# Kernel optimization log

Measured on AMD Instinct MI355X. Metric: run time of the kernel, lower is better.

The kernel has to match this reference:

```python
import jax, jax.numpy as jnp
import numpy as np

EPS = 1e-5  # BatchNorm2d default eps


def _deform_conv(x, offset, W_def, b_def, K):
    # torchvision.ops.DeformConv2d, stride=1, dilation=1, padding=K//2, groups=1
    B, C, H, W = x.shape
    KK = K * K
    pad = K // 2
    # offset channels ordered (y, x) per kernel tap: [B, KK, 2, H, W]
    off = offset.reshape(B, KK, 2, H, W)
    ky = (jnp.arange(KK) // K).astype(x.dtype)
    kx = (jnp.arange(KK) % K).astype(x.dtype)
    base_y = jnp.arange(H, dtype=x.dtype)[None, :, None] - pad + ky[:, None, None]  # [KK,H,1]
    base_x = jnp.arange(W, dtype=x.dtype)[None, None, :] - pad + kx[:, None, None]  # [KK,1,W]
    py = off[:, :, 0] + base_y[None]  # [B,KK,H,W] sampling rows
    px = off[:, :, 1] + base_x[None]  # [B,KK,H,W] sampling cols
    y0 = jnp.floor(py)
    x0 = jnp.floor(px)
    wy = py - y0
    wx = px - x0
    xf = x.reshape(B, C, H * W)

    def corner(iy, ix, w):
        valid = ((iy >= 0) & (iy < H) & (ix >= 0) & (ix < W)).astype(x.dtype)
        idx = jnp.clip(iy, 0, H - 1).astype(jnp.int32) * W + jnp.clip(ix, 0, W - 1).astype(jnp.int32)
        g = jnp.take_along_axis(xf, idx.reshape(B, 1, KK * H * W), axis=2)
        return g.reshape(B, C, KK, H, W) * (w * valid)[:, None]

    sampled = (corner(y0, x0, (1 - wy) * (1 - wx))
               + corner(y0, x0 + 1, (1 - wy) * wx)
               + corner(y0 + 1, x0, wy * (1 - wx))
               + corner(y0 + 1, x0 + 1, wy * wx))  # [B,C,KK,H,W]
    out = jnp.einsum('bckhw,ock->bohw', sampled, W_def.reshape(W_def.shape[0], C, KK))
    return out + b_def[None, :, None, None]


def reference(x, W_off, b_off, W_def, b_def, W_cat, b_cat, gamma, beta):
    K = W_def.shape[-1]
    # 3x3 offset-generating conv, padding=1
    offset = jax.lax.conv_general_dilated(
        x, W_off, (1, 1), ((1, 1), (1, 1)),
        dimension_numbers=('NCHW', 'OIHW', 'NCHW')) + b_off[None, :, None, None]
    y1 = _deform_conv(x, offset, W_def, b_def, K)
    # 1x1 conv
    y = jnp.einsum('bchw,oc->bohw', y1, W_cat) + b_cat[None, :, None, None]
    # BatchNorm2d in training mode (batch statistics, biased var)
    mean = y.mean(axis=(0, 2, 3))
    var = y.var(axis=(0, 2, 3))
    yn = (y - mean[None, :, None, None]) * jax.lax.rsqrt(var + EPS)[None, :, None, None]
    out = jax.nn.relu(gamma[None, :, None, None] * yn + beta[None, :, None, None])
    return out + x


def setup_inputs() -> dict:
    key = jax.random.key(0)
    ks = jax.random.split(key, 5)
    B, C, H, W, K = 4, 64, 192, 192, 3
    return {
        'x': jax.random.normal(ks[0], (B, C, H, W), dtype=jnp.float32),
        'W_off': jax.random.normal(ks[1], (2 * K * K, C, 3, 3), dtype=jnp.float32) * 0.02,
        'b_off': jnp.zeros((2 * K * K,), dtype=jnp.float32),
        'W_def': jax.random.normal(ks[2], (C, C, K, K), dtype=jnp.float32) * (1.0 / np.sqrt(C * K * K)),
        'b_def': jnp.zeros((C,), dtype=jnp.float32),
        'W_cat': jax.random.normal(ks[3], (C, C), dtype=jnp.float32) * (1.0 / np.sqrt(C)),
        'b_cat': jnp.zeros((C,), dtype=jnp.float32),
        'gamma': jnp.ones((C,), dtype=jnp.float32),
        'beta': jnp.zeros((C,), dtype=jnp.float32),
    }
```

## Files before the change

kernel.cpp:

```cpp
#include <hip/hip_runtime.h>
#include <math.h>

constexpr int Hh  = 192;
constexpr int Ww  = 192;
constexpr int HWp = Hh * Ww;
constexpr int Cc  = 64;
constexpr int Bb  = 4;
constexpr int KK  = 9;
constexpr int OFFC = 18;
constexpr int PXB = 32;
constexpr int NBPX = HWp / PXB;
constexpr int KSD = (Cc * KK) / 32;
constexpr int KSC = Cc / 32;
constexpr int NIT = KK * PXB;
constexpr int SLOTS = 64;

using bf16x8 = __attribute__((ext_vector_type(8))) short;
using f32x4  = __attribute__((ext_vector_type(4))) float;

static __device__ __forceinline__ unsigned short f2bf(float f) {
    unsigned int u = __float_as_uint(f);
    u += 0x7fff + ((u >> 16) & 1);
    return (unsigned short)(u >> 16);
}
static __device__ __forceinline__ float bf2f(unsigned short u) {
    return __uint_as_float((unsigned)u << 16);
}

__global__ __launch_bounds__(256)
void k_xpose(const float* __restrict__ x, unsigned short* __restrict__ xcl) {
    __shared__ unsigned short tile[64][66];
    int b   = blockIdx.x / (HWp / 64);
    int px0 = (blockIdx.x % (HWp / 64)) * 64;
    int t = threadIdx.x;
    #pragma unroll
    for (int r = 0; r < 4; ++r) {
        int c = r * 16 + (t >> 4), px4 = (t & 15) * 4;
        float4 v = *(const float4*)(x + ((size_t)b * Cc + c) * HWp + px0 + px4);
        tile[c][px4 + 0] = f2bf(v.x);
        tile[c][px4 + 1] = f2bf(v.y);
        tile[c][px4 + 2] = f2bf(v.z);
        tile[c][px4 + 3] = f2bf(v.w);
    }
    __syncthreads();
    #pragma unroll
    for (int r = 0; r < 4; ++r) {
        int pxl = r * 16 + (t >> 4), c4 = (t & 15) * 4;
        ushort4 u;
        u.x = tile[c4 + 0][pxl];
        u.y = tile[c4 + 1][pxl];
        u.z = tile[c4 + 2][pxl];
        u.w = tile[c4 + 3][pxl];
        *(ushort4*)(xcl + ((size_t)b * HWp + px0 + pxl) * Cc + c4) = u;
    }
}

__global__ __launch_bounds__(256)
void k_wprep(const float* __restrict__ Wdef, const float* __restrict__ Wcat,
             const float* __restrict__ Woff,
             unsigned short* __restrict__ Fd, unsigned short* __restrict__ Fc,
             unsigned short* __restrict__ Fo) {
    int i = blockIdx.x * 256 + threadIdx.x;
    if (i < 4 * KSD * 64 * 8) {
        int r = i & 7, lane = (i >> 3) & 63, ks = (i >> 9) % KSD, ot = (i >> 9) / KSD;
        int o  = ot * 16 + (lane & 15);
        int kp = ks * 32 + ((lane >> 4) << 3) + r;
        int kk = kp >> 6, c = kp & 63;
        Fd[i] = f2bf(Wdef[o * (Cc * KK) + c * KK + kk]);
    }
    int j = i - 4 * KSD * 64 * 8;
    if (j >= 0 && j < 4 * KSC * 64 * 8) {
        int r = j & 7, lane = (j >> 3) & 63, ks = (j >> 9) & 1, ot = j >> 10;
        int o = ot * 16 + (lane & 15);
        int c = ks * 32 + ((lane >> 4) << 3) + r;
        Fc[j] = f2bf(Wcat[o * Cc + c]);
    }
    int m = j - 4 * KSC * 64 * 8;
    if (m >= 0 && m < 2 * KSD * 64 * 8) {
        int r = m & 7, lane = (m >> 3) & 63, ks = (m >> 9) % KSD, ot = (m >> 9) / KSD;
        int o  = ot * 16 + (lane & 15);
        int kp = ks * 32 + ((lane >> 4) << 3) + r;
        int kk = kp >> 6, c = kp & 63;
        Fo[m] = (o < OFFC) ? f2bf(Woff[o * (Cc * KK) + c * KK + kk]) : 0;
    }
}

__global__ __launch_bounds__(256)
void k_fused(const unsigned short* __restrict__ xcl,
             const unsigned short* __restrict__ Fo, const float* __restrict__ boff,
             const unsigned short* __restrict__ Fd, const float* __restrict__ bdef,
             const unsigned short* __restrict__ Fc, const float* __restrict__ bcat,
             float* __restrict__ y, float* __restrict__ psum) {
    __shared__ __align__(16) unsigned char s_buf[PXB * Cc * KK * 2];
    __shared__ __align__(16) unsigned char s_y1[PXB * Cc * 2];
    __shared__ float s_off[PXB][OFFC];
    __shared__ __align__(16) int s_pp[NIT * 8];

    const int t = threadIdx.x;
    const int lane = t & 63, wv = t >> 6;
    const int klane = lane >> 4;
    const int c4 = (lane & 15) * 4;
    int wg = blockIdx.x;
    const int slot = wg & (SLOTS - 1);
    wg = (wg & 7) * (Bb * NBPX / 8) + (wg >> 3);
    const int b   = wg / NBPX;
    const int px0 = (wg % NBPX) * PXB;
    const int h   = px0 / Ww;
    const int w0  = px0 % Ww;
    const unsigned short* xb = xcl + (size_t)b * HWp * Cc;

    #pragma unroll
    for (int it = 0; it < NIT / 16; ++it) {
        int item = it * 16 + wv * 4 + klane;
        int kk = item >> 5, pxl = item & 31;
        int ky = (kk * 11) >> 5, kx = kk - ky * 3;
        int row = h + ky - 1;
        int col = w0 + pxl + kx - 1;
        ushort4 u = {0, 0, 0, 0};
        if (row >= 0 && row < Hh && col >= 0 && col < Ww)
            u = *(const ushort4*)(xb + (size_t)(row * Ww + col) * Cc + c4);
        unsigned addr = (unsigned)pxl * (Cc * KK * 2)
                      + ((((unsigned)(kk * 64 + c4)) * 2) ^ ((unsigned)(pxl & 7) << 4));
        *(ushort4*)(s_buf + addr) = u;
    }
    __syncthreads();

    {
        const int pxt = wv & 1, oto = wv >> 1;
        const unsigned swzA = (unsigned)(lane & 7) << 4;
        const unsigned rA = ((unsigned)(lane & 15) + (unsigned)pxt * 16) * (Cc * KK * 2);
        f32x4 a = {0.f, 0.f, 0.f, 0.f};
        const bf16x8* Bo = (const bf16x8*)Fo + (size_t)oto * KSD * 64;
        #pragma unroll 3
        for (int ks = 0; ks < KSD; ++ks) {
            unsigned cb = ((unsigned)(ks * 64 + klane * 16)) ^ swzA;
            bf16x8 af = *(const bf16x8*)(s_buf + rA + cb);
            a = __builtin_amdgcn_mfma_f32_16x16x32_bf16(af, Bo[ks * 64 + lane], a, 0, 0, 0);
        }
        int oc = oto * 16 + (lane & 15);
        if (oc < OFFC) {
            float bv = boff[oc];
            #pragma unroll
            for (int r = 0; r < 4; ++r)
                s_off[pxt * 16 + klane * 4 + r][oc] = a[r] + bv;
        }
    }
    __syncthreads();

    for (int i = t; i < NIT; i += 256) {
        int kk = i >> 5, pxl = i & 31;
        int ky = (kk * 11) >> 5, kx = kk - ky * 3;
        float py  = s_off[pxl][kk * 2]     + (float)(h - 1 + ky);
        float pxf = s_off[pxl][kk * 2 + 1] + (float)(w0 + pxl - 1 + kx);
        float fy0 = floorf(py), fx0 = floorf(pxf);
        float wy = py - fy0, wx = pxf - fx0;
        int iy0 = (int)fy0, ix0 = (int)fx0, iy1 = iy0 + 1, ix1 = ix0 + 1;
        float v00 = (iy0 >= 0 && iy0 < Hh && ix0 >= 0 && ix0 < Ww) ? 1.f : 0.f;
        float v01 = (iy0 >= 0 && iy0 < Hh && ix1 >= 0 && ix1 < Ww) ? 1.f : 0.f;
        float v10 = (iy1 >= 0 && iy1 < Hh && ix0 >= 0 && ix0 < Ww) ? 1.f : 0.f;
        float v11 = (iy1 >= 0 && iy1 < Hh && ix1 >= 0 && ix1 < Ww) ? 1.f : 0.f;
        int cy0 = min(max(iy0, 0), Hh - 1), cy1 = min(max(iy1, 0), Hh - 1);
        int cx0 = min(max(ix0, 0), Ww - 1), cx1 = min(max(ix1, 0), Ww - 1);
        int* pp = &s_pp[i * 8];
        pp[0] = (cy0 * Ww + cx0) * (Cc * 2);
        pp[1] = (cy0 * Ww + cx1) * (Cc * 2);
        pp[2] = (cy1 * Ww + cx0) * (Cc * 2);
        pp[3] = (cy1 * Ww + cx1) * (Cc * 2);
        pp[4] = __float_as_int((1.f - wy) * (1.f - wx) * v00);
        pp[5] = __float_as_int((1.f - wy) * wx * v01);
        pp[6] = __float_as_int(wy * (1.f - wx) * v10);
        pp[7] = __float_as_int(wy * wx * v11);
    }
    __syncthreads();

    const unsigned char* xbB = (const unsigned char*)xb + (size_t)c4 * 2;
    #pragma unroll 2
    for (int it = 0; it < NIT / 16; ++it) {
        int item = it * 16 + wv * 4 + klane;
        int kk = item >> 5, pxl = item & 31;
        const int* pp = &s_pp[item * 8];
        int4   idx = *(const int4*)pp;
        float4 wt  = *(const float4*)(pp + 4);
        ushort4 u00 = *(const ushort4*)(xbB + idx.x);
        ushort4 u01 = *(const ushort4*)(xbB + idx.y);
        ushort4 u10 = *(const ushort4*)(xbB + idx.z);
        ushort4 u11 = *(const ushort4*)(xbB + idx.w);
        float v0 = wt.x * bf2f(u00.x) + wt.y * bf2f(u01.x) + wt.z * bf2f(u10.x) + wt.w * bf2f(u11.x);
        float v1 = wt.x * bf2f(u00.y) + wt.y * bf2f(u01.y) + wt.z * bf2f(u10.y) + wt.w * bf2f(u11.y);
        float v2 = wt.x * bf2f(u00.z) + wt.y * bf2f(u01.z) + wt.z * bf2f(u10.z) + wt.w * bf2f(u11.z);
        float v3 = wt.x * bf2f(u00.w) + wt.y * bf2f(u01.w) + wt.z * bf2f(u10.w) + wt.w * bf2f(u11.w);
        ushort4 o4;
        o4.x = f2bf(v0); o4.y = f2bf(v1); o4.z = f2bf(v2); o4.w = f2bf(v3);
        unsigned addr = (unsigned)pxl * (Cc * KK * 2)
                      + ((((unsigned)(kk * 64 + c4)) * 2) ^ ((unsigned)(pxl & 7) << 4));
        *(ushort4*)(s_buf + addr) = o4;
    }
    __syncthreads();

    const int ot = wv;
    const unsigned swzA = (unsigned)(lane & 7) << 4;
    const unsigned rA0  = (unsigned)(lane & 15) * (Cc * KK * 2);
    const unsigned rA1  = rA0 + 16u * (Cc * KK * 2);
    f32x4 acc0 = {0.f, 0.f, 0.f, 0.f}, acc1 = {0.f, 0.f, 0.f, 0.f};
    const bf16x8* Bd = (const bf16x8*)Fd + (size_t)ot * KSD * 64;
    #pragma unroll 3
    for (int ks = 0; ks < KSD; ++ks) {
        unsigned cb = ((unsigned)(ks * 64 + klane * 16)) ^ swzA;
        bf16x8 a0 = *(const bf16x8*)(s_buf + rA0 + cb);
        bf16x8 a1 = *(const bf16x8*)(s_buf + rA1 + cb);
        bf16x8 bd = Bd[ks * 64 + lane];
        acc0 = __builtin_amdgcn_mfma_f32_16x16x32_bf16(a0, bd, acc0, 0, 0, 0);
        acc1 = __builtin_amdgcn_mfma_f32_16x16x32_bf16(a1, bd, acc1, 0, 0, 0);
    }
    const int o = ot * 16 + (lane & 15);
    {
        float bv = bdef[o];
        unsigned colb = (unsigned)o * 2;
        #pragma unroll
        for (int r = 0; r < 4; ++r) {
            int row0 = klane * 4 + r, row1 = row0 + 16;
            unsigned sw = (unsigned)(row0 & 7) << 4;
            *(unsigned short*)(s_y1 + row0 * (Cc * 2) + (colb ^ sw)) = f2bf(acc0[r] + bv);
            *(unsigned short*)(s_y1 + row1 * (Cc * 2) + (colb ^ sw)) = f2bf(acc1[r] + bv);
        }
    }
    __syncthreads();

    f32x4 c0 = {0.f, 0.f, 0.f, 0.f}, c1 = {0.f, 0.f, 0.f, 0.f};
    const bf16x8* Bc = (const bf16x8*)Fc + (size_t)ot * KSC * 64;
    const unsigned rY0 = (unsigned)(lane & 15) * (Cc * 2);
    const unsigned rY1 = rY0 + 16u * (Cc * 2);
    #pragma unroll
    for (int ks = 0; ks < KSC; ++ks) {
        unsigned cb = ((unsigned)(ks * 64 + klane * 16)) ^ swzA;
        bf16x8 a0 = *(const bf16x8*)(s_y1 + rY0 + cb);
        bf16x8 a1 = *(const bf16x8*)(s_y1 + rY1 + cb);
        bf16x8 bc = Bc[ks * 64 + lane];
        c0 = __builtin_amdgcn_mfma_f32_16x16x32_bf16(a0, bc, c0, 0, 0, 0);
        c1 = __builtin_amdgcn_mfma_f32_16x16x32_bf16(a1, bc, c1, 0, 0, 0);
    }

    float vals[8];
    {
        float bcv = bcat[o];
        #pragma unroll
        for (int r = 0; r < 4; ++r) { vals[r] = c0[r] + bcv; vals[4 + r] = c1[r] + bcv; }
        float s1 = 0.f, s2 = 0.f;
        #pragma unroll
        for (int j = 0; j < 8; ++j) { s1 += vals[j]; s2 += vals[j] * vals[j]; }
        s1 += __shfl_xor(s1, 16); s1 += __shfl_xor(s1, 32);
        s2 += __shfl_xor(s2, 16); s2 += __shfl_xor(s2, 32);
        if (klane == 0) {
            atomicAdd(&psum[o * SLOTS + slot], s1);
            atomicAdd(&psum[Cc * SLOTS + o * SLOTS + slot], s2);
        }
    }

    __syncthreads();
    {
        unsigned orow = (unsigned)o * (PXB * 4);
        unsigned sw   = (unsigned)(o & 7) << 4;
        #pragma unroll
        for (int r = 0; r < 4; ++r) {
            int p0 = klane * 4 + r, p1 = p0 + 16;
            *(float*)(s_buf + orow + (((unsigned)p0 * 4) ^ sw)) = vals[r];
            *(float*)(s_buf + orow + (((unsigned)p1 * 4) ^ sw)) = vals[4 + r];
        }
    }
    __syncthreads();
    float* yb = y + (size_t)b * Cc * HWp + px0;
    #pragma unroll
    for (int it = 0; it < 2; ++it) {
        int oo = it * 32 + (t >> 3), pxq = t & 7;
        float4 v = *(const float4*)(s_buf + (unsigned)oo * (PXB * 4)
                                    + (((unsigned)pxq * 16) ^ ((unsigned)(oo & 7) << 4)));
        *(float4*)(yb + (size_t)oo * HWp + pxq * 4) = v;
    }
}

__global__ __launch_bounds__(64)
void k_stats_final(const float* __restrict__ psum, float* __restrict__ stats) {
    int c = threadIdx.x;
    double t1 = 0.0, t2 = 0.0;
    for (int s = 0; s < SLOTS; ++s) {
        t1 += (double)psum[c * SLOTS + s];
        t2 += (double)psum[Cc * SLOTS + c * SLOTS + s];
    }
    double n = (double)(Bb * HWp);
    double mean = t1 / n;
    double var  = t2 / n - mean * mean;
    stats[c]      = (float)mean;
    stats[Cc + c] = (float)(1.0 / sqrt(var + 1e-5));
}

__global__ __launch_bounds__(256)
void k_apply(const float4* __restrict__ y, const float4* __restrict__ x,
             const float* __restrict__ stats, const float* __restrict__ gamma,
             const float* __restrict__ beta, float4* __restrict__ out) {
    int idx = blockIdx.x * 256 + threadIdx.x;
    int c = (idx / (HWp / 4)) % Cc;
    float mean = stats[c], inv = stats[Cc + c];
    float g = gamma[c], bt = beta[c];
    float4 yv = y[idx], xv = x[idx], o;
    o.x = fmaxf(g * ((yv.x - mean) * inv) + bt, 0.f) + xv.x;
    o.y = fmaxf(g * ((yv.y - mean) * inv) + bt, 0.f) + xv.y;
    o.z = fmaxf(g * ((yv.z - mean) * inv) + bt, 0.f) + xv.z;
    o.w = fmaxf(g * ((yv.w - mean) * inv) + bt, 0.f) + xv.w;
    out[idx] = o;
}

extern "C" void kernel_launch(void* const* d_in, const int* in_sizes, int n_in,
                              void* d_out, int out_size, void* d_ws, size_t ws_size,
                              hipStream_t stream) {
    const float* x     = (const float*)d_in[0];
    const float* Woff  = (const float*)d_in[1];
    const float* boff  = (const float*)d_in[2];
    const float* Wdef  = (const float*)d_in[3];
    const float* bdef  = (const float*)d_in[4];
    const float* Wcat  = (const float*)d_in[5];
    const float* bcat  = (const float*)d_in[6];
    const float* gamma = (const float*)d_in[7];
    const float* beta  = (const float*)d_in[8];
    float* out = (float*)d_out;

    float* ws    = (float*)d_ws;
    float* ybuf  = ws;
    float* stats = ybuf + (size_t)Bb * Cc * HWp;
    float* psum  = stats + 128;
    unsigned short* Fd  = (unsigned short*)(psum + 2 * Cc * SLOTS);
    unsigned short* Fc  = Fd + 4 * KSD * 64 * 8;
    unsigned short* Fo  = Fc + 4 * KSC * 64 * 8;
    unsigned short* xcl = Fo + 2 * KSD * 64 * 8;

    hipMemsetAsync(psum, 0, 2 * Cc * SLOTS * sizeof(float), stream);
    k_xpose<<<dim3(Bb * (HWp / 64)), dim3(256), 0, stream>>>(x, xcl);
    k_wprep<<<dim3((4 * KSD * 64 * 8 + 4 * KSC * 64 * 8 + 2 * KSD * 64 * 8 + 255) / 256),
              dim3(256), 0, stream>>>(Wdef, Wcat, Woff, Fd, Fc, Fo);
    k_fused<<<dim3(Bb * NBPX), dim3(256), 0, stream>>>(xcl, Fo, boff, Fd, bdef, Fc, bcat, ybuf, psum);
    k_stats_final<<<dim3(1), dim3(64), 0, stream>>>(psum, stats);
    k_apply<<<dim3(Bb * Cc * HWp / 4 / 256), dim3(256), 0, stream>>>(
        (const float4*)ybuf, (const float4*)x, stats, gamma, beta, (float4*)out);
}
```

Baseline: 217.5 us.

## Merge prep kernels, widen fused block to 512 threads, store intermediate y in bf16

Three changes at once. The transpose, weight-prep and psum-zeroing launches are merged into one kernel, dropping a memset and a launch. The fused kernel now runs 8 waves per block, so each wave does one 16x16 output tile instead of two. The pre-BatchNorm activation y is written and read as bf16 instead of fp32, halving that round-trip through memory. The trade-offs are lower precision in the normalised output, since the stats still come from fp32 values, and higher register and occupancy pressure at 512 threads.

```diff
diff --git a/kernel.cpp b/kernel.cpp
--- a/kernel.cpp
+++ b/kernel.cpp
@@ -15,6 +15,10 @@
 constexpr int NIT = KK * PXB;
 constexpr int SLOTS = 64;
 
+constexpr int NXP = Bb * (HWp / 64);
+constexpr int NWP = (4 * KSD * 64 * 8 + 4 * KSC * 64 * 8 + 2 * KSD * 64 * 8) / 256;
+constexpr int NZP = (2 * Cc * SLOTS / 4) / 256;
+
 using bf16x8 = __attribute__((ext_vector_type(8))) short;
 using f32x4  = __attribute__((ext_vector_type(4))) float;
 
@@ -28,69 +32,74 @@
 }
 
 __global__ __launch_bounds__(256)
-void k_xpose(const float* __restrict__ x, unsigned short* __restrict__ xcl) {
+void k_prep(const float* __restrict__ x, const float* __restrict__ Wdef,
+            const float* __restrict__ Wcat, const float* __restrict__ Woff,
+            unsigned short* __restrict__ xcl, unsigned short* __restrict__ Fd,
+            unsigned short* __restrict__ Fc, unsigned short* __restrict__ Fo,
+            float* __restrict__ psum) {
     __shared__ unsigned short tile[64][66];
-    int b   = blockIdx.x / (HWp / 64);
-    int px0 = (blockIdx.x % (HWp / 64)) * 64;
-    int t = threadIdx.x;
-    #pragma unroll
-    for (int r = 0; r < 4; ++r) {
-        int c = r * 16 + (t >> 4), px4 = (t & 15) * 4;
-        float4 v = *(const float4*)(x + ((size_t)b * Cc + c) * HWp + px0 + px4);
-        tile[c][px4 + 0] = f2bf(v.x);
-        tile[c][px4 + 1] = f2bf(v.y);
-        tile[c][px4 + 2] = f2bf(v.z);
-        tile[c][px4 + 3] = f2bf(v.w);
-    }
-    __syncthreads();
-    #pragma unroll
-    for (int r = 0; r < 4; ++r) {
-        int pxl = r * 16 + (t >> 4), c4 = (t & 15) * 4;
-        ushort4 u;
-        u.x = tile[c4 + 0][pxl];
-        u.y = tile[c4 + 1][pxl];
-        u.z = tile[c4 + 2][pxl];
-        u.w = tile[c4 + 3][pxl];
-        *(ushort4*)(xcl + ((size_t)b * HWp + px0 + pxl) * Cc + c4) = u;
-    }
-}
-
-__global__ __launch_bounds__(256)
-void k_wprep(const float* __restrict__ Wdef, const float* __restrict__ Wcat,
-             const float* __restrict__ Woff,
-             unsigned short* __restrict__ Fd, unsigned short* __restrict__ Fc,
-             unsigned short* __restrict__ Fo) {
-    int i = blockIdx.x * 256 + threadIdx.x;
-    if (i < 4 * KSD * 64 * 8) {
-        int r = i & 7, lane = (i >> 3) & 63, ks = (i >> 9) % KSD, ot = (i >> 9) / KSD;
-        int o  = ot * 16 + (lane & 15);
-        int kp = ks * 32 + ((lane >> 4) << 3) + r;
-        int kk = kp >> 6, c = kp & 63;
-        Fd[i] = f2bf(Wdef[o * (Cc * KK) + c * KK + kk]);
-    }
-    int j = i - 4 * KSD * 64 * 8;
-    if (j >= 0 && j < 4 * KSC * 64 * 8) {
-        int r = j & 7, lane = (j >> 3) & 63, ks = (j >> 9) & 1, ot = j >> 10;
-        int o = ot * 16 + (lane & 15);
-        int c = ks * 32 + ((lane >> 4) << 3) + r;
-        Fc[j] = f2bf(Wcat[o * Cc + c]);
-    }
-    int m = j - 4 * KSC * 64 * 8;
-    if (m >= 0 && m < 2 * KSD * 64 * 8) {
-        int r = m & 7, lane = (m >> 3) & 63, ks = (m >> 9) % KSD, ot = (m >> 9) / KSD;
-        int o  = ot * 16 + (lane & 15);
-        int kp = ks * 32 + ((lane >> 4) << 3) + r;
-        int kk = kp >> 6, c = kp & 63;
-        Fo[m] = (o < OFFC) ? f2bf(Woff[o * (Cc * KK) + c * KK + kk]) : 0;
-    }
-}
-
-__global__ __launch_bounds__(256)
+    const int bid = blockIdx.x;
+    const int t = threadIdx.x;
+    if (bid < NXP) {
+        int b   = bid / (HWp / 64);
+        int px0 = (bid % (HWp / 64)) * 64;
+        #pragma unroll
+        for (int r = 0; r < 4; ++r) {
+            int c = r * 16 + (t >> 4), px4 = (t & 15) * 4;
+            float4 v = *(const float4*)(x + ((size_t)b * Cc + c) * HWp + px0 + px4);
+            tile[c][px4 + 0] = f2bf(v.x);
+            tile[c][px4 + 1] = f2bf(v.y);
+            tile[c][px4 + 2] = f2bf(v.z);
+            tile[c][px4 + 3] = f2bf(v.w);
+        }
+        __syncthreads();
+        #pragma unroll
+        for (int r = 0; r < 4; ++r) {
+            int pxl = r * 16 + (t >> 4), c4 = (t & 15) * 4;
+            ushort4 u;
+            u.x = tile[c4 + 0][pxl];
+            u.y = tile[c4 + 1][pxl];
+            u.z = tile[c4 + 2][pxl];
+            u.w = tile[c4 + 3][pxl];
+            *(ushort4*)(xcl + ((size_t)b * HWp + px0 + pxl) * Cc + c4) = u;
+        }
+    } else if (bid < NXP + NWP) {
+        int i = (bid - NXP) * 256 + t;
+        if (i < 4 * KSD * 64 * 8) {
+            int r = i & 7, lane = (i >> 3) & 63, ks = (i >> 9) % KSD, ot = (i >> 9) / KSD;
+            int o  = ot * 16 + (lane & 15);
+            int kp = ks * 32 + ((lane >> 4) << 3) + r;
+            int kk = kp >> 6, c = kp & 63;
+            Fd[i] = f2bf(Wdef[o * (Cc * KK) + c * KK + kk]);
+        }
+        int j = i - 4 * KSD * 64 * 8;
+        if (j >= 0 && j < 4 * KSC * 64 * 8) {
+            int r = j & 7, lane = (j >> 3) & 63, ks = (j >> 9) & 1, ot = j >> 10;
+            int o = ot * 16 + (lane & 15);
+            int c = ks * 32 + ((lane >> 4) << 3) + r;
+            Fc[j] = f2bf(Wcat[o * Cc + c]);
+        }
+        int m = j - 4 * KSC * 64 * 8;
+        if (m >= 0 && m < 2 * KSD * 64 * 8) {
+            int r = m & 7, lane = (m >> 3) & 63, ks = (m >> 9) % KSD, ot = (m >> 9) / KSD;
+            int o  = ot * 16 + (lane & 15);
+            int kp = ks * 32 + ((lane >> 4) << 3) + r;
+            int kk = kp >> 6, c = kp & 63;
+            Fo[m] = (o < OFFC) ? f2bf(Woff[o * (Cc * KK) + c * KK + kk]) : 0;
+        }
+    } else {
+        int j = (bid - NXP - NWP) * 256 + t;
+        float4 z = {0.f, 0.f, 0.f, 0.f};
+        ((float4*)psum)[j] = z;
+    }
+}
+
+__global__ __launch_bounds__(512)
 void k_fused(const unsigned short* __restrict__ xcl,
              const unsigned short* __restrict__ Fo, const float* __restrict__ boff,
              const unsigned short* __restrict__ Fd, const float* __restrict__ bdef,
              const unsigned short* __restrict__ Fc, const float* __restrict__ bcat,
-             float* __restrict__ y, float* __restrict__ psum) {
+             unsigned short* __restrict__ y, float* __restrict__ psum) {
     __shared__ __align__(16) unsigned char s_buf[PXB * Cc * KK * 2];
     __shared__ __align__(16) unsigned char s_y1[PXB * Cc * 2];
     __shared__ float s_off[PXB][OFFC];
@@ -98,7 +107,7 @@
 
     const int t = threadIdx.x;
     const int lane = t & 63, wv = t >> 6;
-    const int klane = lane >> 4;
+    const int klane = (lane >> 4) & 3;
     const int c4 = (lane & 15) * 4;
     int wg = blockIdx.x;
     const int slot = wg & (SLOTS - 1);
@@ -110,8 +119,8 @@
     const unsigned short* xb = xcl + (size_t)b * HWp * Cc;
 
     #pragma unroll
-    for (int it = 0; it < NIT / 16; ++it) {
-        int item = it * 16 + wv * 4 + klane;
+    for (int it = 0; it < NIT / 32; ++it) {
+        int item = it * 32 + wv * 4 + klane;
         int kk = item >> 5, pxl = item & 31;
         int ky = (kk * 11) >> 5, kx = kk - ky * 3;
         int row = h + ky - 1;
@@ -125,15 +134,15 @@
     }
     __syncthreads();
 
-    {
-        const int pxt = wv & 1, oto = wv >> 1;
-        const unsigned swzA = (unsigned)(lane & 7) << 4;
+    if (wv < 4) {
+        const int oto = wv >> 1, pxt = wv & 1;
+        const unsigned swz = (unsigned)(lane & 7) << 4;
         const unsigned rA = ((unsigned)(lane & 15) + (unsigned)pxt * 16) * (Cc * KK * 2);
         f32x4 a = {0.f, 0.f, 0.f, 0.f};
         const bf16x8* Bo = (const bf16x8*)Fo + (size_t)oto * KSD * 64;
         #pragma unroll 3
         for (int ks = 0; ks < KSD; ++ks) {
-            unsigned cb = ((unsigned)(ks * 64 + klane * 16)) ^ swzA;
+            unsigned cb = ((unsigned)(ks * 64 + klane * 16)) ^ swz;
             bf16x8 af = *(const bf16x8*)(s_buf + rA + cb);
             a = __builtin_amdgcn_mfma_f32_16x16x32_bf16(af, Bo[ks * 64 + lane], a, 0, 0, 0);
         }
@@ -147,7 +156,8 @@
     }
     __syncthreads();
 
-    for (int i = t; i < NIT; i += 256) {
+    if (t < NIT) {
+        int i = t;
         int kk = i >> 5, pxl = i & 31;
         int ky = (kk * 11) >> 5, kx = kk - ky * 3;
         float py  = s_off[pxl][kk * 2]     + (float)(h - 1 + ky);
@@ -174,9 +184,9 @@
     __syncthreads();
 
     const unsigned char* xbB = (const unsigned char*)xb + (size_t)c4 * 2;
-    #pragma unroll 2
-    for (int it = 0; it < NIT / 16; ++it) {
-        int item = it * 16 + wv * 4 + klane;
+    #pragma unroll 3
+    for (int it = 0; it < NIT / 32; ++it) {
+        int item = it * 32 + wv * 4 + klane;
         int kk = item >> 5, pxl = item & 31;
         const int* pp = &s_pp[item * 8];
         int4   idx = *(const int4*)pp;
@@ -197,20 +207,17 @@
     }
     __syncthreads();
 
-    const int ot = wv;
+    const int ot = wv >> 1, pxt = wv & 1;
     const unsigned swzA = (unsigned)(lane & 7) << 4;
-    const unsigned rA0  = (unsigned)(lane & 15) * (Cc * KK * 2);
-    const unsigned rA1  = rA0 + 16u * (Cc * KK * 2);
-    f32x4 acc0 = {0.f, 0.f, 0.f, 0.f}, acc1 = {0.f, 0.f, 0.f, 0.f};
+    const unsigned rA = ((unsigned)(lane & 15) + (unsigned)pxt * 16) * (Cc * KK * 2);
+    f32x4 acc = {0.f, 0.f, 0.f, 0.f};
     const bf16x8* Bd = (const bf16x8*)Fd + (size_t)ot * KSD * 64;
     #pragma unroll 3
     for (int ks = 0; ks < KSD; ++ks) {
         unsigned cb = ((unsigned)(ks * 64 + klane * 16)) ^ swzA;
-        bf16x8 a0 = *(const bf16x8*)(s_buf + rA0 + cb);
-        bf16x8 a1 = *(const bf16x8*)(s_buf + rA1 + cb);
+        bf16x8 a0 = *(const bf16x8*)(s_buf + rA + cb);
         bf16x8 bd = Bd[ks * 64 + lane];
-        acc0 = __builtin_amdgcn_mfma_f32_16x16x32_bf16(a0, bd, acc0, 0, 0, 0);
-        acc1 = __builtin_amdgcn_mfma_f32_16x16x32_bf16(a1, bd, acc1, 0, 0, 0);
+        acc = __builtin_amdgcn_mfma_f32_16x16x32_bf16(a0, bd, acc, 0, 0, 0);
     }
     const int o = ot * 16 + (lane & 15);
     {
@@ -218,36 +225,32 @@
         unsigned colb = (unsigned)o * 2;
         #pragma unroll
         for (int r = 0; r < 4; ++r) {
-            int row0 = klane * 4 + r, row1 = row0 + 16;
-            unsigned sw = (unsigned)(row0 & 7) << 4;
-            *(unsigned short*)(s_y1 + row0 * (Cc * 2) + (colb ^ sw)) = f2bf(acc0[r] + bv);
-            *(unsigned short*)(s_y1 + row1 * (Cc * 2) + (colb ^ sw)) = f2bf(acc1[r] + bv);
-        }
-    }
-    __syncthreads();
-
-    f32x4 c0 = {0.f, 0.f, 0.f, 0.f}, c1 = {0.f, 0.f, 0.f, 0.f};
+            int row = pxt * 16 + klane * 4 + r;
+            unsigned sw = (unsigned)((klane * 4 + r) & 7) << 4;
+            *(unsigned short*)(s_y1 + row * (Cc * 2) + (colb ^ sw)) = f2bf(acc[r] + bv);
+        }
+    }
+    __syncthreads();
+
+    f32x4 cacc = {0.f, 0.f, 0.f, 0.f};
     const bf16x8* Bc = (const bf16x8*)Fc + (size_t)ot * KSC * 64;
-    const unsigned rY0 = (unsigned)(lane & 15) * (Cc * 2);
-    const unsigned rY1 = rY0 + 16u * (Cc * 2);
+    const unsigned rY = ((unsigned)(lane & 15) + (unsigned)pxt * 16) * (Cc * 2);
     #pragma unroll
     for (int ks = 0; ks < KSC; ++ks) {
         unsigned cb = ((unsigned)(ks * 64 + klane * 16)) ^ swzA;
-        bf16x8 a0 = *(const bf16x8*)(s_y1 + rY0 + cb);
-        bf16x8 a1 = *(const bf16x8*)(s_y1 + rY1 + cb);
+        bf16x8 a0 = *(const bf16x8*)(s_y1 + rY + cb);
         bf16x8 bc = Bc[ks * 64 + lane];
-        c0 = __builtin_amdgcn_mfma_f32_16x16x32_bf16(a0, bc, c0, 0, 0, 0);
-        c1 = __builtin_amdgcn_mfma_f32_16x16x32_bf16(a1, bc, c1, 0, 0, 0);
-    }
-
-    float vals[8];
+        cacc = __builtin_amdgcn_mfma_f32_16x16x32_bf16(a0, bc, cacc, 0, 0, 0);
+    }
+
+    float vals[4];
     {
         float bcv = bcat[o];
         #pragma unroll
-        for (int r = 0; r < 4; ++r) { vals[r] = c0[r] + bcv; vals[4 + r] = c1[r] + bcv; }
+        for (int r = 0; r < 4; ++r) vals[r] = cacc[r] + bcv;
         float s1 = 0.f, s2 = 0.f;
         #pragma unroll
-        for (int j = 0; j < 8; ++j) { s1 += vals[j]; s2 += vals[j] * vals[j]; }
+        for (int j = 0; j < 4; ++j) { s1 += vals[j]; s2 += vals[j] * vals[j]; }
         s1 += __shfl_xor(s1, 16); s1 += __shfl_xor(s1, 32);
         s2 += __shfl_xor(s2, 16); s2 += __shfl_xor(s2, 32);
         if (klane == 0) {
@@ -262,19 +265,19 @@
         unsigned sw   = (unsigned)(o & 7) << 4;
         #pragma unroll
         for (int r = 0; r < 4; ++r) {
-            int p0 = klane * 4 + r, p1 = p0 + 16;
-            *(float*)(s_buf + orow + (((unsigned)p0 * 4) ^ sw)) = vals[r];
-            *(float*)(s_buf + orow + (((unsigned)p1 * 4) ^ sw)) = vals[4 + r];
-        }
-    }
-    __syncthreads();
-    float* yb = y + (size_t)b * Cc * HWp + px0;
-    #pragma unroll
-    for (int it = 0; it < 2; ++it) {
-        int oo = it * 32 + (t >> 3), pxq = t & 7;
+            int p = pxt * 16 + klane * 4 + r;
+            *(float*)(s_buf + orow + (((unsigned)p * 4) ^ sw)) = vals[r];
+        }
+    }
+    __syncthreads();
+    unsigned short* yb = y + (size_t)b * Cc * HWp + px0;
+    {
+        int oo = t >> 3, pxq = t & 7;
         float4 v = *(const float4*)(s_buf + (unsigned)oo * (PXB * 4)
                                     + (((unsigned)pxq * 16) ^ ((unsigned)(oo & 7) << 4)));
-        *(float4*)(yb + (size_t)oo * HWp + pxq * 4) = v;
+        ushort4 u;
+        u.x = f2bf(v.x); u.y = f2bf(v.y); u.z = f2bf(v.z); u.w = f2bf(v.w);
+        *(ushort4*)(yb + (size_t)oo * HWp + pxq * 4) = u;
     }
 }
 
@@ -294,18 +297,19 @@
 }
 
 __global__ __launch_bounds__(256)
-void k_apply(const float4* __restrict__ y, const float4* __restrict__ x,
+void k_apply(const unsigned short* __restrict__ y, const float4* __restrict__ x,
              const float* __restrict__ stats, const float* __restrict__ gamma,
              const float* __restrict__ beta, float4* __restrict__ out) {
     int idx = blockIdx.x * 256 + threadIdx.x;
     int c = (idx / (HWp / 4)) % Cc;
     float mean = stats[c], inv = stats[Cc + c];
     float g = gamma[c], bt = beta[c];
-    float4 yv = y[idx], xv = x[idx], o;
-    o.x = fmaxf(g * ((yv.x - mean) * inv) + bt, 0.f) + xv.x;
-    o.y = fmaxf(g * ((yv.y - mean) * inv) + bt, 0.f) + xv.y;
-    o.z = fmaxf(g * ((yv.z - mean) * inv) + bt, 0.f) + xv.z;
-    o.w = fmaxf(g * ((yv.w - mean) * inv) + bt, 0.f) + xv.w;
+    ushort4 yv = *(const ushort4*)(y + (size_t)idx * 4);
+    float4 xv = x[idx], o;
+    o.x = fmaxf(g * ((bf2f(yv.x) - mean) * inv) + bt, 0.f) + xv.x;
+    o.y = fmaxf(g * ((bf2f(yv.y) - mean) * inv) + bt, 0.f) + xv.y;
+    o.z = fmaxf(g * ((bf2f(yv.z) - mean) * inv) + bt, 0.f) + xv.z;
+    o.w = fmaxf(g * ((bf2f(yv.w) - mean) * inv) + bt, 0.f) + xv.w;
     out[idx] = o;
 }
 
@@ -324,20 +328,18 @@
     float* out = (float*)d_out;
 
     float* ws    = (float*)d_ws;
-    float* ybuf  = ws;
-    float* stats = ybuf + (size_t)Bb * Cc * HWp;
+    float* stats = ws;
     float* psum  = stats + 128;
-    unsigned short* Fd  = (unsigned short*)(psum + 2 * Cc * SLOTS);
+    unsigned short* y16 = (unsigned short*)(psum + 2 * Cc * SLOTS);
+    unsigned short* Fd  = y16 + (size_t)Bb * Cc * HWp;
     unsigned short* Fc  = Fd + 4 * KSD * 64 * 8;
     unsigned short* Fo  = Fc + 4 * KSC * 64 * 8;
     unsigned short* xcl = Fo + 2 * KSD * 64 * 8;
 
-    hipMemsetAsync(psum, 0, 2 * Cc * SLOTS * sizeof(float), stream);
-    k_xpose<<<dim3(Bb * (HWp / 64)), dim3(256), 0, stream>>>(x, xcl);
-    k_wprep<<<dim3((4 * KSD * 64 * 8 + 4 * KSC * 64 * 8 + 2 * KSD * 64 * 8 + 255) / 256),
-              dim3(256), 0, stream>>>(Wdef, Wcat, Woff, Fd, Fc, Fo);
-    k_fused<<<dim3(Bb * NBPX), dim3(256), 0, stream>>>(xcl, Fo, boff, Fd, bdef, Fc, bcat, ybuf, psum);
+    k_prep<<<dim3(NXP + NWP + NZP), dim3(256), 0, stream>>>(x, Wdef, Wcat, Woff,
+                                                            xcl, Fd, Fc, Fo, psum);
+    k_fused<<<dim3(Bb * NBPX), dim3(512), 0, stream>>>(xcl, Fo, boff, Fd, bdef, Fc, bcat, y16, psum);
     k_stats_final<<<dim3(1), dim3(64), 0, stream>>>(psum, stats);
     k_apply<<<dim3(Bb * Cc * HWp / 4 / 256), dim3(256), 0, stream>>>(
-        (const float4*)ybuf, (const float4*)x, stats, gamma, beta, (float4*)out);
-}
+        y16, (const float4*)x, stats, gamma, beta, (float4*)out);
+}
```

Result: slower. 221.9 us (+2.0%).
